# Kernel tuning notes

Measured on AMD Instinct MI355X. Metric: run time of the kernel, lower is better.

Reference implementation:

```python
import jax, jax.numpy as jnp
import numpy as np

S = 14       # grid size
B = 2        # boxes per cell
C = 20       # classes
N_EL = B * 5 + C   # 30
L_COORD = 5.0
L_NOOBJ = 0.5
BATCH = 4096
NBOX = 16


def setup_inputs() -> dict:
    key = jax.random.key(0)
    k1, k2, k3, k4 = jax.random.split(key, 4)
    prediction = jax.random.uniform(k1, (BATCH, S * S * N_EL), dtype=jnp.float32)
    # well-formed ground-truth boxes: centers in (0.05,0.95), sizes in (0.02,0.3)
    cxcy = jax.random.uniform(k2, (BATCH, NBOX, 2), minval=0.05, maxval=0.95, dtype=jnp.float32)
    wh = jax.random.uniform(k3, (BATCH, NBOX, 2), minval=0.02, maxval=0.3, dtype=jnp.float32)
    boxes = jnp.concatenate([cxcy - wh / 2, cxcy + wh / 2], axis=-1)  # x1,y1,x2,y2
    classes = jax.random.randint(k4, (BATCH, NBOX), 0, C, dtype=jnp.int32)
    return {"prediction": prediction, "boxes": boxes, "classes": classes}


def _encode(boxes, classes):
    """Vectorized version of YoloLoss.encode: scatter boxes into SxS grid cells.
    Faithful detail: class one-hot goes to channel 9+class (the original's
    off-by-one: class 0 lands on the 2nd confidence channel)."""
    bsz, nbox = classes.shape
    cell = 1.0 / S
    xy1, xy2 = boxes[..., :2], boxes[..., 2:]
    wh = xy2 - xy1
    cxcy = (xy1 + xy2) / 2
    ij = jnp.clip(jnp.ceil(cxcy / cell) - 1, 0, S - 1)          # [b,nbox,2] (x,y)
    dxy = cxcy / cell - ij                                      # delta inside cell
    ij = ij.astype(jnp.int32)
    one = jnp.ones_like(wh[..., :1])
    zcls = jnp.zeros(classes.shape + (C,), dtype=boxes.dtype)
    # layout: [dxy, wh, conf, dxy, wh, conf, class one-hots]
    base = jnp.concatenate([dxy, wh, one, dxy, wh, one, zcls], axis=-1)  # [b,nbox,30]
    cls_oh = jax.nn.one_hot(classes + (B * 5 - 1), N_EL, dtype=boxes.dtype)  # index 9+class
    vec = jnp.maximum(base, cls_oh)
    flat_idx = (jnp.arange(bsz, dtype=jnp.int32)[:, None] * (S * S)
                + ij[..., 1] * S + ij[..., 0]).reshape(-1)      # row-major (y,x)
    target = jnp.zeros((bsz * S * S, N_EL), dtype=boxes.dtype)
    return target.at[flat_idx].set(vec.reshape(-1, N_EL))


def _pairwise_iou(a, b):
    """a,b: [N,B,4] -> iou [N,B(pred),B(target)] (corner-format jaccard, as in
    the original, applied to (dx,dy,w,h) rows verbatim)."""
    a4 = a[:, :, None, :]
    b4 = b[:, None, :, :]
    lt = jnp.maximum(a4[..., :2], b4[..., :2])
    rb = jnp.minimum(a4[..., 2:], b4[..., 2:])
    whi = jnp.clip(rb - lt, 0.0)
    inter = whi[..., 0] * whi[..., 1]
    area_a = (a4[..., 2] - a4[..., 0]) * (a4[..., 3] - a4[..., 1])
    area_b = (b4[..., 2] - b4[..., 0]) * (b4[..., 3] - b4[..., 1])
    union = area_a + area_b - inter
    return inter / jnp.where(union == 0, 1.0, union)


def reference(prediction, boxes, classes):
    target = _encode(boxes, classes)                       # [bsz*S*S, 30]
    pred = prediction.reshape(-1, N_EL)
    coord = target[:, 4] > 0                               # cells containing objects
    coordf = coord.astype(pred.dtype)
    noobjf = (target[:, 4] == 0).astype(pred.dtype)

    conf_idx = jnp.array([4, 9])
    noobj_loss = jnp.sum(noobjf[:, None] * (pred[:, conf_idx] - target[:, conf_idx]) ** 2)
    class_loss = jnp.sum(coordf[:, None] * (pred[:, B * 5:] - target[:, B * 5:]) ** 2)

    bp = pred[:, :B * 5].reshape(-1, B, 5)                 # [N,B,5]
    bt = target[:, :B * 5].reshape(-1, B, 5)

    iou = _pairwise_iou(bp[..., :4], bt[..., :4])          # [N,B,B]
    max_index = jnp.argmax(iou, axis=1)                    # best pred per target box
    response = (max_index[:, None, :] == jnp.arange(B)[None, :, None]).any(-1)  # [N,B]
    resp = response & coord[:, None]
    respf = resp.astype(pred.dtype)

    contain_loss = jnp.sum(respf * (bp[..., 4] - bt[..., 4]) ** 2)
    bt_wh = jnp.where(resp[..., None], bt[..., 2:4], 1.0)  # guard sqrt at masked cells
    loc_loss = jnp.sum(respf * (((bp[..., :2] - bt[..., :2]) ** 2).sum(-1)
                                + ((jnp.sqrt(bp[..., 2:4]) - jnp.sqrt(bt_wh)) ** 2).sum(-1)))

    return L_COORD * loc_loss + contain_loss + L_NOOBJ * noobj_loss + class_loss
```

## Files before the change

kernel.cpp:

```cpp
#include <hip/hip_runtime.h>


#define SGRID 14
#define CELLS 196
#define NEL 30
#define NBOX 16
#define PRED_PER_BATCH (CELLS * NEL)

__global__ __launch_bounds__(256) void yolo_loss_kernel(
    const float* __restrict__ pred,
    const float* __restrict__ boxes,
    const int*   __restrict__ classes,
    float* __restrict__ out)
{
    __shared__ float s_pred[PRED_PER_BATCH];
    __shared__ float s_dx[NBOX], s_dy[NBOX], s_w[NBOX], s_h[NBOX];
    __shared__ int   s_cell[NBOX], s_cls[NBOX];
    __shared__ float s_wsum[4];

    const int batch = blockIdx.x;
    const int tid   = threadIdx.x;

    {
        const float4* src = (const float4*)(pred + (size_t)batch * PRED_PER_BATCH);
        float4* dst = (float4*)s_pred;
        #pragma unroll
        for (int i = 0; i < PRED_PER_BATCH / 4 / 256 + 1; ++i) {
            int idx = tid + i * 256;
            if (idx < PRED_PER_BATCH / 4) dst[idx] = src[idx];
        }
    }

    if (tid < NBOX) {
        const float* b = boxes + ((size_t)batch * NBOX + tid) * 4;
        float x1 = b[0], y1 = b[1], x2 = b[2], y2 = b[3];
        const float cellw = (float)(1.0 / 14.0);
        float w  = x2 - x1,            h  = y2 - y1;
        float cx = (x1 + x2) * 0.5f,   cy = (y1 + y2) * 0.5f;
        float fx = cx / cellw,         fy = cy / cellw;
        float fi = fminf(fmaxf(ceilf(fx) - 1.0f, 0.0f), 13.0f);
        float fj = fminf(fmaxf(ceilf(fy) - 1.0f, 0.0f), 13.0f);
        s_dx[tid]   = fx - fi;
        s_dy[tid]   = fy - fj;
        s_w[tid]    = w;
        s_h[tid]    = h;
        s_cell[tid] = (int)fj * SGRID + (int)fi;
        s_cls[tid]  = classes[batch * NBOX + tid];
    }
    __syncthreads();

    float loss = 0.0f;
    if (tid < CELLS) {
        int k = -1;
        #pragma unroll
        for (int b = 0; b < NBOX; ++b)
            if (s_cell[b] == tid) k = b;

        const float* p = s_pred + tid * NEL;
        if (k < 0) {
            loss = 0.5f * (p[4] * p[4] + p[9] * p[9]);
        } else {
            const float dx = s_dx[k], dy = s_dy[k];
            const float w  = s_w[k],  h  = s_h[k];
            const int cls  = s_cls[k];

            const int hot = 9 + cls;
            #pragma unroll
            for (int c = 10; c < 30; ++c) {
                float t = (c == hot) ? 1.0f : 0.0f;
                float d = p[c] - t;
                loss += d * d;
            }

            float iou[2];
            const float area_t = (w - dx) * (h - dy);
            #pragma unroll
            for (int i = 0; i < 2; ++i) {
                const float* a = p + i * 5;
                float ltx = fmaxf(a[0], dx), lty = fmaxf(a[1], dy);
                float rbx = fminf(a[2], w),  rby = fminf(a[3], h);
                float wi = fmaxf(rbx - ltx, 0.0f);
                float hi = fmaxf(rby - lty, 0.0f);
                float inter  = wi * hi;
                float area_a = (a[2] - a[0]) * (a[3] - a[1]);
                float uni    = area_a + area_t - inter;
                iou[i] = inter / ((uni == 0.0f) ? 1.0f : uni);
            }
            int r = (iou[1] > iou[0]) ? 1 : 0;
            const float* a = p + r * 5;

            float dc = a[4] - 1.0f;
            loss += dc * dc;

            float lx = a[0] - dx;
            float ly = a[1] - dy;
            float lw = sqrtf(a[2]) - sqrtf(w);
            float lh = sqrtf(a[3]) - sqrtf(h);
            loss += 5.0f * (lx * lx + ly * ly + lw * lw + lh * lh);
        }
    }

    #pragma unroll
    for (int off = 32; off > 0; off >>= 1)
        loss += __shfl_down(loss, off, 64);
    const int wave = tid >> 6;
    if ((tid & 63) == 0) s_wsum[wave] = loss;
    __syncthreads();
    if (tid == 0) {
        float tot = s_wsum[0] + s_wsum[1] + s_wsum[2] + s_wsum[3];
        atomicAdd(out, tot);
    }
}

extern "C" void kernel_launch(void* const* d_in, const int* in_sizes, int n_in,
                              void* d_out, int out_size, void* d_ws, size_t ws_size,
                              hipStream_t stream) {
    const float* pred    = (const float*)d_in[0];
    const float* boxes   = (const float*)d_in[1];
    const int*   classes = (const int*)d_in[2];
    float* out = (float*)d_out;

    const int batch = in_sizes[0] / PRED_PER_BATCH;

    hipMemsetAsync(d_out, 0, sizeof(float) * out_size, stream);

    yolo_loss_kernel<<<dim3(batch), dim3(256), 0, stream>>>(pred, boxes, classes, out);
}
```

Measured before the change: 177.7 us.

## Split YOLO loss into encode, per-cell main, and final reduce kernels

Replaces the one-block-per-batch kernel, which staged each 23 KB prediction slab through shared memory, with three kernels. A box-encode kernel scatters box winners per cell via atomicMax into a workspace grid. A flat per-cell kernel then reads predictions directly from global memory, loading all 30 channels only for object cells. A single-block kernel reduces per-wave partials, replacing the global atomicAdd. This frees shared memory for occupancy and skips most prediction loads, at the cost of extra launches, a workspace memset and uncoalesced strided per-thread reads.

```diff
diff --git a/kernel.cpp b/kernel.cpp
--- a/kernel.cpp
+++ b/kernel.cpp
@@ -7,76 +7,70 @@
 #define NBOX 16
 #define PRED_PER_BATCH (CELLS * NEL)
 
-__global__ __launch_bounds__(256) void yolo_loss_kernel(
+__global__ void encode_kernel(const float* __restrict__ boxes,
+                              const int*   __restrict__ classes,
+                              int*   __restrict__ winner,
+                              float* __restrict__ params,
+                              int nbb)
+{
+    int t = blockIdx.x * blockDim.x + threadIdx.x;
+    if (t >= nbb) return;
+    int b = t >> 4;
+    int k = t & 15;
+    float4 bx = ((const float4*)boxes)[t];
+    float w  = bx.z - bx.x,  h  = bx.w - bx.y;
+    float cx = (bx.x + bx.z) * 0.5f, cy = (bx.y + bx.w) * 0.5f;
+    const float cellw = (float)(1.0 / 14.0);
+    float fx = cx / cellw, fy = cy / cellw;
+    float fi = fminf(fmaxf(ceilf(fx) - 1.0f, 0.0f), 13.0f);
+    float fj = fminf(fmaxf(ceilf(fy) - 1.0f, 0.0f), 13.0f);
+    int cell = (int)fj * SGRID + (int)fi;
+    float* pr = params + (size_t)t * 8;
+    pr[0] = fx - fi;  pr[1] = fy - fj;
+    pr[2] = w;        pr[3] = h;
+    pr[4] = (float)classes[t];
+    atomicMax(&winner[b * CELLS + cell], k);
+}
+
+__global__ __launch_bounds__(256) void yolo_main_kernel(
     const float* __restrict__ pred,
-    const float* __restrict__ boxes,
-    const int*   __restrict__ classes,
-    float* __restrict__ out)
+    const int*   __restrict__ winner,
+    const float* __restrict__ params,
+    float* __restrict__ partials,
+    int total)
 {
-    __shared__ float s_pred[PRED_PER_BATCH];
-    __shared__ float s_dx[NBOX], s_dy[NBOX], s_w[NBOX], s_h[NBOX];
-    __shared__ int   s_cell[NBOX], s_cls[NBOX];
-    __shared__ float s_wsum[4];
+    int idx = blockIdx.x * 256 + threadIdx.x;
+    float loss = 0.0f;
+    if (idx < total) {
+        int b    = idx / CELLS;
+        const float* p = pred + (size_t)idx * NEL;
+        int k = winner[idx];
+        if (k < 0) {
+            float2 a = *(const float2*)(p + 4);
+            float2 c = *(const float2*)(p + 8);
+            loss = 0.5f * (a.x * a.x + c.y * c.y);
+        } else {
+            float pp[NEL];
+            #pragma unroll
+            for (int j = 0; j < NEL / 2; ++j)
+                ((float2*)pp)[j] = ((const float2*)p)[j];
+            const float* pr = params + (size_t)(b * NBOX + k) * 8;
+            float dx = pr[0], dy = pr[1], w = pr[2], h = pr[3];
+            int cls = (int)pr[4];
 
-    const int batch = blockIdx.x;
-    const int tid   = threadIdx.x;
-
-    {
-        const float4* src = (const float4*)(pred + (size_t)batch * PRED_PER_BATCH);
-        float4* dst = (float4*)s_pred;
-        #pragma unroll
-        for (int i = 0; i < PRED_PER_BATCH / 4 / 256 + 1; ++i) {
-            int idx = tid + i * 256;
-            if (idx < PRED_PER_BATCH / 4) dst[idx] = src[idx];
-        }
-    }
-
-    if (tid < NBOX) {
-        const float* b = boxes + ((size_t)batch * NBOX + tid) * 4;
-        float x1 = b[0], y1 = b[1], x2 = b[2], y2 = b[3];
-        const float cellw = (float)(1.0 / 14.0);
-        float w  = x2 - x1,            h  = y2 - y1;
-        float cx = (x1 + x2) * 0.5f,   cy = (y1 + y2) * 0.5f;
-        float fx = cx / cellw,         fy = cy / cellw;
-        float fi = fminf(fmaxf(ceilf(fx) - 1.0f, 0.0f), 13.0f);
-        float fj = fminf(fmaxf(ceilf(fy) - 1.0f, 0.0f), 13.0f);
-        s_dx[tid]   = fx - fi;
-        s_dy[tid]   = fy - fj;
-        s_w[tid]    = w;
-        s_h[tid]    = h;
-        s_cell[tid] = (int)fj * SGRID + (int)fi;
-        s_cls[tid]  = classes[batch * NBOX + tid];
-    }
-    __syncthreads();
-
-    float loss = 0.0f;
-    if (tid < CELLS) {
-        int k = -1;
-        #pragma unroll
-        for (int b = 0; b < NBOX; ++b)
-            if (s_cell[b] == tid) k = b;
-
-        const float* p = s_pred + tid * NEL;
-        if (k < 0) {
-            loss = 0.5f * (p[4] * p[4] + p[9] * p[9]);
-        } else {
-            const float dx = s_dx[k], dy = s_dy[k];
-            const float w  = s_w[k],  h  = s_h[k];
-            const int cls  = s_cls[k];
-
-            const int hot = 9 + cls;
+            int hot = 9 + cls;
             #pragma unroll
-            for (int c = 10; c < 30; ++c) {
+            for (int c = 10; c < NEL; ++c) {
                 float t = (c == hot) ? 1.0f : 0.0f;
-                float d = p[c] - t;
+                float d = pp[c] - t;
                 loss += d * d;
             }
 
+            float area_t = (w - dx) * (h - dy);
             float iou[2];
-            const float area_t = (w - dx) * (h - dy);
             #pragma unroll
             for (int i = 0; i < 2; ++i) {
-                const float* a = p + i * 5;
+                const float* a = pp + i * 5;
                 float ltx = fmaxf(a[0], dx), lty = fmaxf(a[1], dy);
                 float rbx = fminf(a[2], w),  rby = fminf(a[3], h);
                 float wi = fmaxf(rbx - ltx, 0.0f);
@@ -87,11 +81,10 @@
                 iou[i] = inter / ((uni == 0.0f) ? 1.0f : uni);
             }
             int r = (iou[1] > iou[0]) ? 1 : 0;
-            const float* a = p + r * 5;
+            const float* a = pp + r * 5;
 
             float dc = a[4] - 1.0f;
             loss += dc * dc;
-
             float lx = a[0] - dx;
             float ly = a[1] - dy;
             float lw = sqrtf(a[2]) - sqrtf(w);
@@ -103,13 +96,22 @@
     #pragma unroll
     for (int off = 32; off > 0; off >>= 1)
         loss += __shfl_down(loss, off, 64);
-    const int wave = tid >> 6;
-    if ((tid & 63) == 0) s_wsum[wave] = loss;
+    if ((threadIdx.x & 63) == 0)
+        partials[(blockIdx.x * 256 + threadIdx.x) >> 6] = loss;
+}
+
+__global__ __launch_bounds__(256) void reduce_kernel(
+    const float* __restrict__ partials, float* __restrict__ out, int n)
+{
+    float s = 0.0f;
+    for (int i = threadIdx.x; i < n; i += 256) s += partials[i];
+    #pragma unroll
+    for (int off = 32; off > 0; off >>= 1)
+        s += __shfl_down(s, off, 64);
+    __shared__ float w4[4];
+    if ((threadIdx.x & 63) == 0) w4[threadIdx.x >> 6] = s;
     __syncthreads();
-    if (tid == 0) {
-        float tot = s_wsum[0] + s_wsum[1] + s_wsum[2] + s_wsum[3];
-        atomicAdd(out, tot);
-    }
+    if (threadIdx.x == 0) out[0] = w4[0] + w4[1] + w4[2] + w4[3];
 }
 
 extern "C" void kernel_launch(void* const* d_in, const int* in_sizes, int n_in,
@@ -121,8 +123,19 @@
     float* out = (float*)d_out;
 
     const int batch = in_sizes[0] / PRED_PER_BATCH;
+    const int total = batch * CELLS;
+    const int nbb   = batch * NBOX;
 
-    hipMemsetAsync(d_out, 0, sizeof(float) * out_size, stream);
+    int*   winner   = (int*)d_ws;
+    float* params   = (float*)((char*)d_ws + (size_t)total * sizeof(int));
+    float* partials = params + (size_t)nbb * 8;
+    const int mgrid  = (total + 255) / 256;
+    const int nwaves = mgrid * 4;
 
-    yolo_loss_kernel<<<dim3(batch), dim3(256), 0, stream>>>(pred, boxes, classes, out);
+    hipMemsetAsync(winner, 0xFF, (size_t)total * sizeof(int), stream);
+    encode_kernel<<<dim3((nbb + 255) / 256), dim3(256), 0, stream>>>(
+        boxes, classes, winner, params, nbb);
+    yolo_main_kernel<<<dim3(mgrid), dim3(256), 0, stream>>>(
+        pred, winner, params, partials, total);
+    reduce_kernel<<<dim3(1), dim3(256), 0, stream>>>(partials, out, nwaves);
 }
```

Result: faster. 159.1 us (-10.5%).
